# Kernel optimization log

Hardware: AMD Instinct MI355X
Metric: run time of the kernel (lower is better)

## Reference

```python
import jax, jax.numpy as jnp
import numpy as np

N, E = 50000, 800000
IN_DIM, HID, OUT, HEADS = 128, 128, 64, 4
C1 = HID // HEADS  # 32 per-head channels in gat1
NEG_SLOPE = 0.2


def _gat_conv(x, src, dst, W, a_src, a_dst, b, heads, ch):
    """PyG GATConv (inference): gather -> edge attention -> segment softmax -> scatter."""
    n = x.shape[0]
    h = (x @ W).reshape(n, heads, ch)                      # [N,H,C]
    alpha_src = jnp.einsum('nhc,hc->nh', h, a_src)         # [N,H]
    alpha_dst = jnp.einsum('nhc,hc->nh', h, a_dst)         # [N,H]
    e = jax.nn.leaky_relu(alpha_src[src] + alpha_dst[dst], NEG_SLOPE)  # [E,H]
    m = jax.ops.segment_max(e, dst, num_segments=n)        # per-target max (stable softmax)
    e = jnp.exp(e - m[dst])
    denom = jax.ops.segment_sum(e, dst, num_segments=n)
    alpha = e / (denom[dst] + 1e-16)                       # [E,H]
    out = jax.ops.segment_sum(h[src] * alpha[:, :, None], dst, num_segments=n)  # [N,H,C]
    return out.reshape(n, heads * ch) + b


def setup_inputs() -> dict:
    key = jax.random.key(0)
    ks = jax.random.split(key, 16)
    x = jax.random.normal(ks[0], (N, IN_DIM), dtype=jnp.float32)
    edge_index = jax.random.randint(ks[1], (2, E), 0, N, dtype=jnp.int64)
    s = lambda fan_in: 1.0 / np.sqrt(fan_in)
    return {
        'x': x,
        'edge_index': edge_index,
        'W1': jax.random.normal(ks[2], (IN_DIM, HEADS * C1), jnp.float32) * s(IN_DIM),
        'a_src1': jax.random.normal(ks[3], (HEADS, C1), jnp.float32) * s(C1),
        'a_dst1': jax.random.normal(ks[4], (HEADS, C1), jnp.float32) * s(C1),
        'b1': jnp.zeros((HID,), jnp.float32),
        'W2': jax.random.normal(ks[5], (HID, OUT), jnp.float32) * s(HID),
        'a_src2': jax.random.normal(ks[6], (1, OUT), jnp.float32) * s(OUT),
        'a_dst2': jax.random.normal(ks[7], (1, OUT), jnp.float32) * s(OUT),
        'b2': jnp.zeros((OUT,), jnp.float32),
        'pw1': jax.random.normal(ks[8], (OUT, OUT), jnp.float32) * s(OUT),
        'pb1': jnp.zeros((OUT,), jnp.float32),
        'pw2': jax.random.normal(ks[9], (OUT, OUT), jnp.float32) * s(OUT),
        'pb2': jnp.zeros((OUT,), jnp.float32),
    }


def reference(x, edge_index, W1, a_src1, a_dst1, b1, W2, a_src2, a_dst2, b2, pw1, pb1, pw2, pb2):
    n = x.shape[0]
    # PyG GATConv add_self_loops=True
    loops = jnp.arange(n, dtype=edge_index.dtype)
    src = jnp.concatenate([edge_index[0], loops])
    dst = jnp.concatenate([edge_index[1], loops])
    h = jax.nn.elu(_gat_conv(x, src, dst, W1, a_src1, a_dst1, b1, HEADS, C1))
    h = jax.nn.elu(_gat_conv(h, src, dst, W2, a_src2, a_dst2, b2, 1, OUT))
    # origin_proj: Linear -> ReLU -> Linear
    h = jax.nn.relu(h @ pw1 + pb1)
    return h @ pw2 + pb2
```

## Files before the change

kernel.cpp:

```cpp
#include <hip/hip_runtime.h>
#include <math.h>

#define N_NODES 50000
#define N_EDGES 800000
#define ET (N_EDGES + N_NODES)
#define IN_DIM 128
#define HID 128
#define OUT_DIM 64
#define BW 64
#define NBUCK ((N_NODES + BW - 1) / BW)
#define NBLK 256
#define EPB 3328
#define NT64 ((N_NODES + 63) / 64)
#define NT32 ((N_NODES + 31) / 32)

typedef __attribute__((ext_vector_type(8))) short bf16x8;
typedef __attribute__((ext_vector_type(4))) float f32x4;

__device__ __forceinline__ float lrelu(float x){ return x >= 0.f ? x : 0.2f * x; }
__device__ __forceinline__ float eluf(float x){ return x > 0.f ? x : expm1f(x); }
__device__ __forceinline__ unsigned f2bf(float f){
    unsigned u = __float_as_uint(f);
    return (u + 0x7fffu + ((u >> 16) & 1u)) >> 16;
}
__device__ __forceinline__ float bflo(unsigned u){ return __uint_as_float(u << 16); }
__device__ __forceinline__ float bfhi(unsigned u){ return __uint_as_float(u & 0xffff0000u); }

__global__ __launch_bounds__(256) void k_count(const int* __restrict__ dst,
                                               int* __restrict__ C,
                                               int* __restrict__ bsum2)
{
    __shared__ int cnt[NBUCK];
    const int tid = threadIdx.x, blk = blockIdx.x;
    for (int i = tid; i < NBUCK; i += 256) cnt[i] = 0;
    __syncthreads();
    #pragma unroll
    for (int j = 0; j < EPB / 256; j++) {
        const int e = blk * EPB + j * 256 + tid;
        if (e < ET) {
            const int d = (e < N_EDGES) ? dst[e] : (e - N_EDGES);
            atomicAdd(&cnt[d >> 6], 1);
        }
    }
    __syncthreads();
    for (int b = tid; b < NBUCK; b += 256) {
        const int v = cnt[b];
        C[b * NBLK + blk] = v;
        if (v) atomicAdd(&bsum2[b], v);
    }
}

__global__ __launch_bounds__(1024) void k_bscanB(const int* __restrict__ bsum2, int* __restrict__ boff2)
{
    __shared__ int part[1024];
    const int t = threadIdx.x;
    int v = (t < NBUCK) ? bsum2[t] : 0;
    part[t] = v;
    __syncthreads();
    #pragma unroll
    for (int d = 1; d < 1024; d <<= 1) {
        int add = (t >= d) ? part[t - d] : 0;
        __syncthreads();
        part[t] += add;
        __syncthreads();
    }
    if (t < NBUCK) boff2[t] = part[t] - v;
    if (t == 0) boff2[NBUCK] = ET;
}

__global__ __launch_bounds__(256) void k_cscanC(const int* __restrict__ C,
                                                const int* __restrict__ boff2,
                                                int* __restrict__ Cs)
{
    __shared__ int part[256];
    const int t = threadIdx.x, b = blockIdx.x;
    int v = C[b * NBLK + t];
    part[t] = v;
    __syncthreads();
    #pragma unroll
    for (int d = 1; d < 256; d <<= 1) {
        int add = (t >= d) ? part[t - d] : 0;
        __syncthreads();
        part[t] += add;
        __syncthreads();
    }
    Cs[b * NBLK + t] = boff2[b] + part[t] - v;
}

__global__ __launch_bounds__(256, 2) void k_gemm1_part2(
    const float* __restrict__ x, const float* __restrict__ W1,
    const float* __restrict__ a_s, const float* __restrict__ a_d,
    unsigned* __restrict__ h1b, float* __restrict__ as1, float* __restrict__ ad1,
    const int* __restrict__ src, const int* __restrict__ dst,
    const int* __restrict__ Cs, uint2* __restrict__ part)
{
    __shared__ unsigned smem[128 * 68 + 64 * 68];
    const int tid = threadIdx.x;

    if (blockIdx.x < NT64) {
        unsigned* sWt = smem;
        unsigned* sxb = smem + 128 * 68;
        const int wave = tid >> 6;
        const int lane = tid & 63;
        const int ll   = lane & 15;
        const int quad = lane >> 4;
        const int n0 = blockIdx.x * 64;

        for (int idx = tid; idx < 8192; idx += 256) {
            const int n = idx & 127, kp = idx >> 7;
            const float w0 = W1[(2 * kp) * 128 + n];
            const float w1 = W1[(2 * kp + 1) * 128 + n];
            sWt[n * 68 + kp] = f2bf(w0) | (f2bf(w1) << 16);
        }
        for (int idx = tid; idx < 4096; idx += 256) {
            const int node = idx >> 6, kp = idx & 63;
            const int n = n0 + node;
            unsigned pk = 0;
            if (n < N_NODES) {
                const float x0 = x[n * 128 + 2 * kp];
                const float x1 = x[n * 128 + 2 * kp + 1];
                pk = f2bf(x0) | (f2bf(x1) << 16);
            }
            sxb[node * 68 + kp] = pk;
        }
        __syncthreads();

        f32x4 acc[8];
        #pragma unroll
        for (int t = 0; t < 8; t++) acc[t] = (f32x4){0.f, 0.f, 0.f, 0.f};

        #pragma unroll
        for (int kk = 0; kk < 4; kk++) {
            const int kpo = 16 * kk + 4 * quad;
            const bf16x8 a = *(const bf16x8*)&sxb[(16 * wave + ll) * 68 + kpo];
            #pragma unroll
            for (int t = 0; t < 8; t++) {
                const bf16x8 b = *(const bf16x8*)&sWt[(16 * t + ll) * 68 + kpo];
                acc[t] = __builtin_amdgcn_mfma_f32_16x16x32_bf16(a, b, acc[t], 0, 0, 0);
            }
        }

        float as_v[8], ad_v[8];
        #pragma unroll
        for (int t = 0; t < 8; t++) { as_v[t] = a_s[16 * t + ll]; ad_v[t] = a_d[16 * t + ll]; }
        unsigned short* h1u = (unsigned short*)h1b;
        #pragma unroll
        for (int r = 0; r < 4; r++) {
            const int n = n0 + 16 * wave + 4 * quad + r;
            float ps0 = acc[0][r] * as_v[0] + acc[1][r] * as_v[1];
            float ps1 = acc[2][r] * as_v[2] + acc[3][r] * as_v[3];
            float ps2 = acc[4][r] * as_v[4] + acc[5][r] * as_v[5];
            float ps3 = acc[6][r] * as_v[6] + acc[7][r] * as_v[7];
            float pd0 = acc[0][r] * ad_v[0] + acc[1][r] * ad_v[1];
            float pd1 = acc[2][r] * ad_v[2] + acc[3][r] * ad_v[3];
            float pd2 = acc[4][r] * ad_v[4] + acc[5][r] * ad_v[5];
            float pd3 = acc[6][r] * ad_v[6] + acc[7][r] * ad_v[7];
            #pragma unroll
            for (int off = 1; off < 16; off <<= 1) {
                ps0 += __shfl_xor(ps0, off); ps1 += __shfl_xor(ps1, off);
                ps2 += __shfl_xor(ps2, off); ps3 += __shfl_xor(ps3, off);
                pd0 += __shfl_xor(pd0, off); pd1 += __shfl_xor(pd1, off);
                pd2 += __shfl_xor(pd2, off); pd3 += __shfl_xor(pd3, off);
            }
            if (n < N_NODES) {
                #pragma unroll
                for (int t = 0; t < 8; t++)
                    h1u[n * 128 + 16 * t + ll] = (unsigned short)f2bf(acc[t][r]);
                if (ll == 0) {
                    as1[n * 4 + 0] = ps0; as1[n * 4 + 1] = ps1;
                    as1[n * 4 + 2] = ps2; as1[n * 4 + 3] = ps3;
                    ad1[n * 4 + 0] = pd0; ad1[n * 4 + 1] = pd1;
                    ad1[n * 4 + 2] = pd2; ad1[n * 4 + 3] = pd3;
                }
            }
        }
    } else {
        const int blk = blockIdx.x - NT64;
        int* base = (int*)smem;
        int* cnt  = (int*)smem + NBUCK;
        for (int b = tid; b < NBUCK; b += 256) { base[b] = Cs[b * NBLK + blk]; cnt[b] = 0; }
        __syncthreads();
        #pragma unroll
        for (int j = 0; j < EPB / 256; j++) {
            const int e = blk * EPB + j * 256 + tid;
            if (e < ET) {
                int s, d;
                if (e < N_EDGES) { s = src[e]; d = dst[e]; } else { s = d = e - N_EDGES; }
                const int b = d >> 6;
                const int r = atomicAdd(&cnt[b], 1);
                part[base[b] + r] = make_uint2((unsigned)d, (unsigned)s);
            }
        }
    }
}

__global__ __launch_bounds__(256) void k_scat2(const int* __restrict__ boff2,
                                               const uint2* __restrict__ part,
                                               int* __restrict__ rowptr,
                                               int* __restrict__ csr_src)
{
    __shared__ int cnt64[BW];
    __shared__ int nbase[BW];
    const int b = blockIdx.x, tid = threadIdx.x;
    const int n0 = b * BW;
    const int lo = boff2[b], hi = boff2[b + 1];
    if (tid < BW) cnt64[tid] = 0;
    __syncthreads();
    for (int i = lo + tid; i < hi; i += 256) {
        atomicAdd(&cnt64[part[i].x & (BW - 1)], 1);
    }
    __syncthreads();
    if (tid < BW) {
        int v = cnt64[tid];
        int incl = v;
        #pragma unroll
        for (int off = 1; off < 64; off <<= 1) {
            int t2 = __shfl_up(incl, off);
            if (tid >= off) incl += t2;
        }
        const int excl = incl - v;
        nbase[tid] = excl;
        const int n = n0 + tid;
        if (n < N_NODES) rowptr[n] = lo + excl;
        cnt64[tid] = 0;
    }
    if (b == 0 && tid == 0) rowptr[N_NODES] = ET;
    __syncthreads();
    for (int i = lo + tid; i < hi; i += 256) {
        const uint2 p = part[i];
        const int dn = (int)p.x & (BW - 1);
        const int r = atomicAdd(&cnt64[dn], 1);
        csr_src[lo + nbase[dn] + r] = (int)p.y;
    }
}

__global__ __launch_bounds__(512, 4) void k_aggr1_l2(
    const int* __restrict__ rowptr, const int* __restrict__ csr_src,
    const float* __restrict__ as1, const float* __restrict__ ad1,
    const uint4* __restrict__ h1u4, const float* __restrict__ b1,
    const float* __restrict__ W2, const float* __restrict__ a_s2, const float* __restrict__ a_d2,
    unsigned* __restrict__ h2b, float* __restrict__ as2, float* __restrict__ ad2)
{
    __shared__ unsigned sWt[64 * 68];
    __shared__ unsigned sxb[32 * 68];
    const int tid = threadIdx.x;
    const int n0 = blockIdx.x * 32;

    for (int idx = tid; idx < 4096; idx += 512) {
        const int n = idx & 63, kp = idx >> 6;
        const float w0 = W2[(2 * kp) * 64 + n];
        const float w1 = W2[(2 * kp + 1) * 64 + n];
        sWt[n * 68 + kp] = f2bf(w0) | (f2bf(w1) << 16);
    }

    {
        const int dl = tid >> 4;
        const int c8 = tid & 15;
        const int hd = c8 >> 2;
        const int d = n0 + dl;
        uint4 o = make_uint4(0, 0, 0, 0);
        if (d < N_NODES) {
            const int r0 = rowptr[d], r1 = rowptr[d + 1];
            const float adv = ad1[d * 4 + hd];
            float den = 0.f;
            float acc[8];
            #pragma unroll
            for (int m = 0; m < 8; m++) acc[m] = 0.f;
            int i = r0;
            for (; i + 4 <= r1; i += 4) {
                const int s0 = csr_src[i],     s1 = csr_src[i + 1];
                const int s2 = csr_src[i + 2], s3 = csr_src[i + 3];
                const float e0 = as1[s0 * 4 + hd], e1 = as1[s1 * 4 + hd];
                const float e2 = as1[s2 * 4 + hd], e3 = as1[s3 * 4 + hd];
                const uint4 u0 = h1u4[s0 * 16 + c8];
                const uint4 u1 = h1u4[s1 * 16 + c8];
                const uint4 u2 = h1u4[s2 * 16 + c8];
                const uint4 u3 = h1u4[s3 * 16 + c8];
                const float w0 = expf(lrelu(e0 + adv));
                const float w1 = expf(lrelu(e1 + adv));
                const float w2 = expf(lrelu(e2 + adv));
                const float w3 = expf(lrelu(e3 + adv));
                den += (w0 + w1) + (w2 + w3);
                acc[0] = fmaf(bflo(u0.x), w0, acc[0]); acc[1] = fmaf(bfhi(u0.x), w0, acc[1]);
                acc[2] = fmaf(bflo(u0.y), w0, acc[2]); acc[3] = fmaf(bfhi(u0.y), w0, acc[3]);
                acc[4] = fmaf(bflo(u0.z), w0, acc[4]); acc[5] = fmaf(bfhi(u0.z), w0, acc[5]);
                acc[6] = fmaf(bflo(u0.w), w0, acc[6]); acc[7] = fmaf(bfhi(u0.w), w0, acc[7]);
                acc[0] = fmaf(bflo(u1.x), w1, acc[0]); acc[1] = fmaf(bfhi(u1.x), w1, acc[1]);
                acc[2] = fmaf(bflo(u1.y), w1, acc[2]); acc[3] = fmaf(bfhi(u1.y), w1, acc[3]);
                acc[4] = fmaf(bflo(u1.z), w1, acc[4]); acc[5] = fmaf(bfhi(u1.z), w1, acc[5]);
                acc[6] = fmaf(bflo(u1.w), w1, acc[6]); acc[7] = fmaf(bfhi(u1.w), w1, acc[7]);
                acc[0] = fmaf(bflo(u2.x), w2, acc[0]); acc[1] = fmaf(bfhi(u2.x), w2, acc[1]);
                acc[2] = fmaf(bflo(u2.y), w2, acc[2]); acc[3] = fmaf(bfhi(u2.y), w2, acc[3]);
                acc[4] = fmaf(bflo(u2.z), w2, acc[4]); acc[5] = fmaf(bfhi(u2.z), w2, acc[5]);
                acc[6] = fmaf(bflo(u2.w), w2, acc[6]); acc[7] = fmaf(bfhi(u2.w), w2, acc[7]);
                acc[0] = fmaf(bflo(u3.x), w3, acc[0]); acc[1] = fmaf(bfhi(u3.x), w3, acc[1]);
                acc[2] = fmaf(bflo(u3.y), w3, acc[2]); acc[3] = fmaf(bfhi(u3.y), w3, acc[3]);
                acc[4] = fmaf(bflo(u3.z), w3, acc[4]); acc[5] = fmaf(bfhi(u3.z), w3, acc[5]);
                acc[6] = fmaf(bflo(u3.w), w3, acc[6]); acc[7] = fmaf(bfhi(u3.w), w3, acc[7]);
            }
            for (; i < r1; ++i) {
                const int s = csr_src[i];
                const float w = expf(lrelu(as1[s * 4 + hd] + adv));
                const uint4 u = h1u4[s * 16 + c8];
                den += w;
                acc[0] = fmaf(bflo(u.x), w, acc[0]); acc[1] = fmaf(bfhi(u.x), w, acc[1]);
                acc[2] = fmaf(bflo(u.y), w, acc[2]); acc[3] = fmaf(bfhi(u.y), w, acc[3]);
                acc[4] = fmaf(bflo(u.z), w, acc[4]); acc[5] = fmaf(bfhi(u.z), w, acc[5]);
                acc[6] = fmaf(bflo(u.w), w, acc[6]); acc[7] = fmaf(bfhi(u.w), w, acc[7]);
            }
            const float inv = 1.f / (den + 1e-16f);
            const float4 bA = ((const float4*)b1)[2 * c8];
            const float4 bB = ((const float4*)b1)[2 * c8 + 1];
            const float v0 = eluf(acc[0] * inv + bA.x);
            const float v1 = eluf(acc[1] * inv + bA.y);
            const float v2 = eluf(acc[2] * inv + bA.z);
            const float v3 = eluf(acc[3] * inv + bA.w);
            const float v4 = eluf(acc[4] * inv + bB.x);
            const float v5 = eluf(acc[5] * inv + bB.y);
            const float v6 = eluf(acc[6] * inv + bB.z);
            const float v7 = eluf(acc[7] * inv + bB.w);
            o.x = f2bf(v0) | (f2bf(v1) << 16);
            o.y = f2bf(v2) | (f2bf(v3) << 16);
            o.z = f2bf(v4) | (f2bf(v5) << 16);
            o.w = f2bf(v6) | (f2bf(v7) << 16);
        }
        unsigned* dstp = &sxb[dl * 68 + 4 * c8];
        dstp[0] = o.x; dstp[1] = o.y; dstp[2] = o.z; dstp[3] = o.w;
    }
    __syncthreads();

    if (tid < 128) {
        const int wave = tid >> 6;
        const int lane = tid & 63;
        const int ll   = lane & 15;
        const int quad = lane >> 4;

        f32x4 acc[4];
        #pragma unroll
        for (int t = 0; t < 4; t++) acc[t] = (f32x4){0.f, 0.f, 0.f, 0.f};

        #pragma unroll
        for (int kk = 0; kk < 4; kk++) {
            const int kpo = 16 * kk + 4 * quad;
            const bf16x8 a = *(const bf16x8*)&sxb[(16 * wave + ll) * 68 + kpo];
            #pragma unroll
            for (int t = 0; t < 4; t++) {
                const bf16x8 b = *(const bf16x8*)&sWt[(16 * t + ll) * 68 + kpo];
                acc[t] = __builtin_amdgcn_mfma_f32_16x16x32_bf16(a, b, acc[t], 0, 0, 0);
            }
        }

        float as_v[4], ad_v[4];
        #pragma unroll
        for (int t = 0; t < 4; t++) { as_v[t] = a_s2[16 * t + ll]; ad_v[t] = a_d2[16 * t + ll]; }
        unsigned short* h2u = (unsigned short*)h2b;
        #pragma unroll
        for (int r = 0; r < 4; r++) {
            const int n = n0 + 16 * wave + 4 * quad + r;
            float ps = acc[0][r] * as_v[0] + acc[1][r] * as_v[1]
                     + acc[2][r] * as_v[2] + acc[3][r] * as_v[3];
            float pd = acc[0][r] * ad_v[0] + acc[1][r] * ad_v[1]
                     + acc[2][r] * ad_v[2] + acc[3][r] * ad_v[3];
            #pragma unroll
            for (int off = 1; off < 16; off <<= 1) {
                ps += __shfl_xor(ps, off);
                pd += __shfl_xor(pd, off);
            }
            if (n < N_NODES) {
                #pragma unroll
                for (int t = 0; t < 4; t++)
                    h2u[n * 64 + 16 * t + ll] = (unsigned short)f2bf(acc[t][r]);
                if (ll == 0) { as2[n] = ps; ad2[n] = pd; }
            }
        }
    }
}

__global__ __launch_bounds__(512, 4) void k_tail(
    const int* __restrict__ rowptr, const int* __restrict__ csr_src,
    const float* __restrict__ as2, const float* __restrict__ ad2,
    const uint4* __restrict__ h2u4, const float* __restrict__ b2,
    const float* __restrict__ pw1, const float* __restrict__ pb1,
    const float* __restrict__ pw2, const float* __restrict__ pb2,
    float* __restrict__ out)
{
    __shared__ float sW1[64 * 64];
    __shared__ float sW2[64 * 64];
    __shared__ float sosp[64][68];
    const int tid = threadIdx.x;
    const int n0 = blockIdx.x * 64;

    for (int i = tid; i < 1024; i += 512) {
        ((float4*)sW1)[i] = ((const float4*)pw1)[i];
        ((float4*)sW2)[i] = ((const float4*)pw2)[i];
    }

    {
        const int dl = tid >> 3;
        const int c8 = tid & 7;
        const int d = n0 + dl;
        float acc[8];
        #pragma unroll
        for (int m = 0; m < 8; m++) acc[m] = 0.f;
        float v0 = 0.f, v1 = 0.f, v2 = 0.f, v3 = 0.f;
        float v4 = 0.f, v5 = 0.f, v6 = 0.f, v7 = 0.f;
        if (d < N_NODES) {
            const int r0 = rowptr[d], r1 = rowptr[d + 1];
            const float adv = ad2[d];
            float den = 0.f;
            int i = r0;
            for (; i + 4 <= r1; i += 4) {
                const int s0 = csr_src[i],      s1_ = csr_src[i + 1];
                const int s2_ = csr_src[i + 2], s3_ = csr_src[i + 3];
                const float e0 = as2[s0], e1 = as2[s1_], e2 = as2[s2_], e3 = as2[s3_];
                const uint4 u0 = h2u4[s0  * 8 + c8];
                const uint4 u1 = h2u4[s1_ * 8 + c8];
                const uint4 u2 = h2u4[s2_ * 8 + c8];
                const uint4 u3 = h2u4[s3_ * 8 + c8];
                const float w0 = expf(lrelu(e0 + adv));
                const float w1 = expf(lrelu(e1 + adv));
                const float w2 = expf(lrelu(e2 + adv));
                const float w3 = expf(lrelu(e3 + adv));
                den += (w0 + w1) + (w2 + w3);
                acc[0] = fmaf(bflo(u0.x), w0, acc[0]); acc[1] = fmaf(bfhi(u0.x), w0, acc[1]);
                acc[2] = fmaf(bflo(u0.y), w0, acc[2]); acc[3] = fmaf(bfhi(u0.y), w0, acc[3]);
                acc[4] = fmaf(bflo(u0.z), w0, acc[4]); acc[5] = fmaf(bfhi(u0.z), w0, acc[5]);
                acc[6] = fmaf(bflo(u0.w), w0, acc[6]); acc[7] = fmaf(bfhi(u0.w), w0, acc[7]);
                acc[0] = fmaf(bflo(u1.x), w1, acc[0]); acc[1] = fmaf(bfhi(u1.x), w1, acc[1]);
                acc[2] = fmaf(bflo(u1.y), w1, acc[2]); acc[3] = fmaf(bfhi(u1.y), w1, acc[3]);
                acc[4] = fmaf(bflo(u1.z), w1, acc[4]); acc[5] = fmaf(bfhi(u1.z), w1, acc[5]);
                acc[6] = fmaf(bflo(u1.w), w1, acc[6]); acc[7] = fmaf(bfhi(u1.w), w1, acc[7]);
                acc[0] = fmaf(bflo(u2.x), w2, acc[0]); acc[1] = fmaf(bfhi(u2.x), w2, acc[1]);
                acc[2] = fmaf(bflo(u2.y), w2, acc[2]); acc[3] = fmaf(bfhi(u2.y), w2, acc[3]);
                acc[4] = fmaf(bflo(u2.z), w2, acc[4]); acc[5] = fmaf(bfhi(u2.z), w2, acc[5]);
                acc[6] = fmaf(bflo(u2.w), w2, acc[6]); acc[7] = fmaf(bfhi(u2.w), w2, acc[7]);
                acc[0] = fmaf(bflo(u3.x), w3, acc[0]); acc[1] = fmaf(bfhi(u3.x), w3, acc[1]);
                acc[2] = fmaf(bflo(u3.y), w3, acc[2]); acc[3] = fmaf(bfhi(u3.y), w3, acc[3]);
                acc[4] = fmaf(bflo(u3.z), w3, acc[4]); acc[5] = fmaf(bfhi(u3.z), w3, acc[5]);
                acc[6] = fmaf(bflo(u3.w), w3, acc[6]); acc[7] = fmaf(bfhi(u3.w), w3, acc[7]);
            }
            for (; i < r1; ++i) {
                const int s = csr_src[i];
                const float w = expf(lrelu(as2[s] + adv));
                const uint4 u = h2u4[s * 8 + c8];
                den += w;
                acc[0] = fmaf(bflo(u.x), w, acc[0]); acc[1] = fmaf(bfhi(u.x), w, acc[1]);
                acc[2] = fmaf(bflo(u.y), w, acc[2]); acc[3] = fmaf(bfhi(u.y), w, acc[3]);
                acc[4] = fmaf(bflo(u.z), w, acc[4]); acc[5] = fmaf(bfhi(u.z), w, acc[5]);
                acc[6] = fmaf(bflo(u.w), w, acc[6]); acc[7] = fmaf(bfhi(u.w), w, acc[7]);
            }
            const float inv = 1.f / (den + 1e-16f);
            const float4 bA = ((const float4*)b2)[2 * c8];
            const float4 bB = ((const float4*)b2)[2 * c8 + 1];
            v0 = eluf(acc[0] * inv + bA.x);
            v1 = eluf(acc[1] * inv + bA.y);
            v2 = eluf(acc[2] * inv + bA.z);
            v3 = eluf(acc[3] * inv + bA.w);
            v4 = eluf(acc[4] * inv + bB.x);
            v5 = eluf(acc[5] * inv + bB.y);
            v6 = eluf(acc[6] * inv + bB.z);
            v7 = eluf(acc[7] * inv + bB.w);
        }
        *(float4*)&sosp[dl][8 * c8]     = make_float4(v0, v1, v2, v3);
        *(float4*)&sosp[dl][8 * c8 + 4] = make_float4(v4, v5, v6, v7);
    }
    __syncthreads();

    const int cg = tid & 15;
    const int ng = tid >> 4;
    const float4 pb1_4 = ((const float4*)pb1)[cg];
    const float4 pb2_4 = ((const float4*)pb2)[cg];
    float4 p[2];
    #pragma unroll
    for (int m = 0; m < 2; m++) p[m] = pb1_4;
    #pragma unroll 8
    for (int k = 0; k < 64; k++) {
        const float4 w = *(const float4*)&sW1[k * 64 + 4 * cg];
        #pragma unroll
        for (int m = 0; m < 2; m++) {
            const float xv = sosp[2 * ng + m][k];
            p[m].x = fmaf(xv, w.x, p[m].x);
            p[m].y = fmaf(xv, w.y, p[m].y);
            p[m].z = fmaf(xv, w.z, p[m].z);
            p[m].w = fmaf(xv, w.w, p[m].w);
        }
    }
    __syncthreads();

    #pragma unroll
    for (int m = 0; m < 2; m++) {
        p[m].x = fmaxf(p[m].x, 0.f); p[m].y = fmaxf(p[m].y, 0.f);
        p[m].z = fmaxf(p[m].z, 0.f); p[m].w = fmaxf(p[m].w, 0.f);
        *(float4*)&sosp[2 * ng + m][4 * cg] = p[m];
    }
    __syncthreads();

    float4 o[2];
    #pragma unroll
    for (int m = 0; m < 2; m++) o[m] = pb2_4;
    #pragma unroll 8
    for (int k = 0; k < 64; k++) {
        const float4 w = *(const float4*)&sW2[k * 64 + 4 * cg];
        #pragma unroll
        for (int m = 0; m < 2; m++) {
            const float xv = sosp[2 * ng + m][k];
            o[m].x = fmaf(xv, w.x, o[m].x);
            o[m].y = fmaf(xv, w.y, o[m].y);
            o[m].z = fmaf(xv, w.z, o[m].z);
            o[m].w = fmaf(xv, w.w, o[m].w);
        }
    }
    #pragma unroll
    for (int m = 0; m < 2; m++) {
        const int n = n0 + 2 * ng + m;
        if (n < N_NODES) ((float4*)out)[n * 16 + cg] = o[m];
    }
}

extern "C" void kernel_launch(void* const* d_in, const int* in_sizes, int n_in,
                              void* d_out, int out_size, void* d_ws, size_t ws_size,
                              hipStream_t stream)
{
    const float* x      = (const float*)d_in[0];
    const int*   ei     = (const int*)d_in[1];
    const int*   src    = ei;
    const int*   dst    = ei + N_EDGES;
    const float* W1     = (const float*)d_in[2];
    const float* a_src1 = (const float*)d_in[3];
    const float* a_dst1 = (const float*)d_in[4];
    const float* b1     = (const float*)d_in[5];
    const float* W2     = (const float*)d_in[6];
    const float* a_src2 = (const float*)d_in[7];
    const float* a_dst2 = (const float*)d_in[8];
    const float* b2     = (const float*)d_in[9];
    const float* pw1    = (const float*)d_in[10];
    const float* pb1    = (const float*)d_in[11];
    const float* pw2    = (const float*)d_in[12];
    const float* pb2    = (const float*)d_in[13];

    uint2* part  = (uint2*)d_ws;
    int* ibase   = (int*)(part + ET);
    int* rowptr  = ibase;
    int* C       = rowptr + 50004;
    int* Cs      = C + 200192;
    int* bsum2   = Cs + 200192;
    int* boff2   = bsum2 + 784;
    int* csr_src = boff2 + 784;
    unsigned* h1b = (unsigned*)(csr_src + 850000);
    unsigned* h2b = h1b + 3200000;
    float* fws   = (float*)(h2b + 1600000);
    float* as1   = fws;
    float* ad1   = as1 + 200000;
    float* as2   = ad1 + 200000;
    float* ad2   = as2 + 50000;

    hipMemsetAsync(bsum2, 0, NBUCK * sizeof(int), stream);
    k_count<<<NBLK, 256, 0, stream>>>(dst, C, bsum2);
    k_bscanB<<<1, 1024, 0, stream>>>(bsum2, boff2);
    k_cscanC<<<NBUCK, 256, 0, stream>>>(C, boff2, Cs);

    k_gemm1_part2<<<NT64 + NBLK, 256, 0, stream>>>(x, W1, a_src1, a_dst1,
                                                   h1b, as1, ad1,
                                                   src, dst, Cs, part);
    k_scat2<<<NBUCK, 256, 0, stream>>>(boff2, part, rowptr, csr_src);

    k_aggr1_l2<<<NT32, 512, 0, stream>>>(rowptr, csr_src, as1, ad1,
                                         (const uint4*)h1b, b1,
                                         W2, a_src2, a_dst2, h2b, as2, ad2);

    k_tail<<<NT64, 512, 0, stream>>>(rowptr, csr_src, as2, ad2,
                                     (const uint4*)h2b, b2,
                                     pw1, pb1, pw2, pb2, (float*)d_out);
}
```

Measured before the change: 243.2 us.

## Split layer-1 aggregation from layer-2 GEMM into separate kernels

Unfuses the layer-1 attention aggregation from the layer-2 projection. The aggregation now runs as its own 256-thread kernel, 16 nodes per block with no shared memory, and writes ELU-activated bf16 features to a new workspace buffer. A separate MFMA kernel reads that buffer to do the W2 projection and the attention logits. The aim is to raise occupancy for the latency-bound gather and avoid idle waves during the GEMM. The cost is an extra launch plus a 12.8 MB write and reread of the intermediate.

```diff
diff --git a/kernel.cpp b/kernel.cpp
--- a/kernel.cpp
+++ b/kernel.cpp
@@ -12,7 +12,6 @@
 #define NBLK 256
 #define EPB 3328
 #define NT64 ((N_NODES + 63) / 64)
-#define NT32 ((N_NODES + 31) / 32)
 
 typedef __attribute__((ext_vector_type(8))) short bf16x8;
 typedef __attribute__((ext_vector_type(4))) float f32x4;
@@ -234,144 +233,149 @@
     }
 }
 
-__global__ __launch_bounds__(512, 4) void k_aggr1_l2(
+__global__ __launch_bounds__(256) void k_aggr1(
     const int* __restrict__ rowptr, const int* __restrict__ csr_src,
     const float* __restrict__ as1, const float* __restrict__ ad1,
     const uint4* __restrict__ h1u4, const float* __restrict__ b1,
+    unsigned* __restrict__ hEb)
+{
+    const int d  = blockIdx.x * 16 + (threadIdx.x >> 4);
+    const int c8 = threadIdx.x & 15;
+    const int hd = c8 >> 2;
+    const int r0 = rowptr[d], r1 = rowptr[d + 1];
+    const float adv = ad1[d * 4 + hd];
+    float den = 0.f;
+    float acc[8];
+    #pragma unroll
+    for (int m = 0; m < 8; m++) acc[m] = 0.f;
+    int i = r0;
+    for (; i + 4 <= r1; i += 4) {
+        const int s0 = csr_src[i],     s1 = csr_src[i + 1];
+        const int s2 = csr_src[i + 2], s3 = csr_src[i + 3];
+        const float e0 = as1[s0 * 4 + hd], e1 = as1[s1 * 4 + hd];
+        const float e2 = as1[s2 * 4 + hd], e3 = as1[s3 * 4 + hd];
+        const uint4 u0 = h1u4[s0 * 16 + c8];
+        const uint4 u1 = h1u4[s1 * 16 + c8];
+        const uint4 u2 = h1u4[s2 * 16 + c8];
+        const uint4 u3 = h1u4[s3 * 16 + c8];
+        const float w0 = expf(lrelu(e0 + adv));
+        const float w1 = expf(lrelu(e1 + adv));
+        const float w2 = expf(lrelu(e2 + adv));
+        const float w3 = expf(lrelu(e3 + adv));
+        den += (w0 + w1) + (w2 + w3);
+        acc[0] = fmaf(bflo(u0.x), w0, acc[0]); acc[1] = fmaf(bfhi(u0.x), w0, acc[1]);
+        acc[2] = fmaf(bflo(u0.y), w0, acc[2]); acc[3] = fmaf(bfhi(u0.y), w0, acc[3]);
+        acc[4] = fmaf(bflo(u0.z), w0, acc[4]); acc[5] = fmaf(bfhi(u0.z), w0, acc[5]);
+        acc[6] = fmaf(bflo(u0.w), w0, acc[6]); acc[7] = fmaf(bfhi(u0.w), w0, acc[7]);
+        acc[0] = fmaf(bflo(u1.x), w1, acc[0]); acc[1] = fmaf(bfhi(u1.x), w1, acc[1]);
+        acc[2] = fmaf(bflo(u1.y), w1, acc[2]); acc[3] = fmaf(bfhi(u1.y), w1, acc[3]);
+        acc[4] = fmaf(bflo(u1.z), w1, acc[4]); acc[5] = fmaf(bfhi(u1.z), w1, acc[5]);
+        acc[6] = fmaf(bflo(u1.w), w1, acc[6]); acc[7] = fmaf(bfhi(u1.w), w1, acc[7]);
+        acc[0] = fmaf(bflo(u2.x), w2, acc[0]); acc[1] = fmaf(bfhi(u2.x), w2, acc[1]);
+        acc[2] = fmaf(bflo(u2.y), w2, acc[2]); acc[3] = fmaf(bfhi(u2.y), w2, acc[3]);
+        acc[4] = fmaf(bflo(u2.z), w2, acc[4]); acc[5] = fmaf(bfhi(u2.z), w2, acc[5]);
+        acc[6] = fmaf(bflo(u2.w), w2, acc[6]); acc[7] = fmaf(bfhi(u2.w), w2, acc[7]);
+        acc[0] = fmaf(bflo(u3.x), w3, acc[0]); acc[1] = fmaf(bfhi(u3.x), w3, acc[1]);
+        acc[2] = fmaf(bflo(u3.y), w3, acc[2]); acc[3] = fmaf(bfhi(u3.y), w3, acc[3]);
+        acc[4] = fmaf(bflo(u3.z), w3, acc[4]); acc[5] = fmaf(bfhi(u3.z), w3, acc[5]);
+        acc[6] = fmaf(bflo(u3.w), w3, acc[6]); acc[7] = fmaf(bfhi(u3.w), w3, acc[7]);
+    }
+    for (; i < r1; ++i) {
+        const int s = csr_src[i];
+        const float w = expf(lrelu(as1[s * 4 + hd] + adv));
+        const uint4 u = h1u4[s * 16 + c8];
+        den += w;
+        acc[0] = fmaf(bflo(u.x), w, acc[0]); acc[1] = fmaf(bfhi(u.x), w, acc[1]);
+        acc[2] = fmaf(bflo(u.y), w, acc[2]); acc[3] = fmaf(bfhi(u.y), w, acc[3]);
+        acc[4] = fmaf(bflo(u.z), w, acc[4]); acc[5] = fmaf(bfhi(u.z), w, acc[5]);
+        acc[6] = fmaf(bflo(u.w), w, acc[6]); acc[7] = fmaf(bfhi(u.w), w, acc[7]);
+    }
+    const float inv = 1.f / (den + 1e-16f);
+    const float4 bA = ((const float4*)b1)[2 * c8];
+    const float4 bB = ((const float4*)b1)[2 * c8 + 1];
+    const float v0 = eluf(acc[0] * inv + bA.x);
+    const float v1 = eluf(acc[1] * inv + bA.y);
+    const float v2 = eluf(acc[2] * inv + bA.z);
+    const float v3 = eluf(acc[3] * inv + bA.w);
+    const float v4 = eluf(acc[4] * inv + bB.x);
+    const float v5 = eluf(acc[5] * inv + bB.y);
+    const float v6 = eluf(acc[6] * inv + bB.z);
+    const float v7 = eluf(acc[7] * inv + bB.w);
+    uint4 o;
+    o.x = f2bf(v0) | (f2bf(v1) << 16);
+    o.y = f2bf(v2) | (f2bf(v3) << 16);
+    o.z = f2bf(v4) | (f2bf(v5) << 16);
+    o.w = f2bf(v6) | (f2bf(v7) << 16);
+    ((uint4*)hEb)[d * 16 + c8] = o;
+}
+
+__global__ __launch_bounds__(256, 4) void k_layer2(
+    const unsigned* __restrict__ hEb,
     const float* __restrict__ W2, const float* __restrict__ a_s2, const float* __restrict__ a_d2,
     unsigned* __restrict__ h2b, float* __restrict__ as2, float* __restrict__ ad2)
 {
     __shared__ unsigned sWt[64 * 68];
-    __shared__ unsigned sxb[32 * 68];
+    __shared__ unsigned sxb[64 * 68];
     const int tid = threadIdx.x;
-    const int n0 = blockIdx.x * 32;
-
-    for (int idx = tid; idx < 4096; idx += 512) {
+    const int wave = tid >> 6;
+    const int lane = tid & 63;
+    const int ll   = lane & 15;
+    const int quad = lane >> 4;
+    const int n0 = blockIdx.x * 64;
+
+    for (int idx = tid; idx < 4096; idx += 256) {
         const int n = idx & 63, kp = idx >> 6;
         const float w0 = W2[(2 * kp) * 64 + n];
         const float w1 = W2[(2 * kp + 1) * 64 + n];
         sWt[n * 68 + kp] = f2bf(w0) | (f2bf(w1) << 16);
     }
-
-    {
-        const int dl = tid >> 4;
-        const int c8 = tid & 15;
-        const int hd = c8 >> 2;
-        const int d = n0 + dl;
-        uint4 o = make_uint4(0, 0, 0, 0);
-        if (d < N_NODES) {
-            const int r0 = rowptr[d], r1 = rowptr[d + 1];
-            const float adv = ad1[d * 4 + hd];
-            float den = 0.f;
-            float acc[8];
+    const uint4* hE4 = (const uint4*)hEb;
+    for (int idx = tid; idx < 1024; idx += 256) {
+        const int node = idx >> 4, q = idx & 15;
+        const int n = n0 + node;
+        uint4 pk = make_uint4(0, 0, 0, 0);
+        if (n < N_NODES) pk = hE4[n * 16 + q];
+        unsigned* dstp = &sxb[node * 68 + 4 * q];
+        dstp[0] = pk.x; dstp[1] = pk.y; dstp[2] = pk.z; dstp[3] = pk.w;
+    }
+    __syncthreads();
+
+    f32x4 acc[4];
+    #pragma unroll
+    for (int t = 0; t < 4; t++) acc[t] = (f32x4){0.f, 0.f, 0.f, 0.f};
+
+    #pragma unroll
+    for (int kk = 0; kk < 4; kk++) {
+        const int kpo = 16 * kk + 4 * quad;
+        const bf16x8 a = *(const bf16x8*)&sxb[(16 * wave + ll) * 68 + kpo];
+        #pragma unroll
+        for (int t = 0; t < 4; t++) {
+            const bf16x8 b = *(const bf16x8*)&sWt[(16 * t + ll) * 68 + kpo];
+            acc[t] = __builtin_amdgcn_mfma_f32_16x16x32_bf16(a, b, acc[t], 0, 0, 0);
+        }
+    }
+
+    float as_v[4], ad_v[4];
+    #pragma unroll
+    for (int t = 0; t < 4; t++) { as_v[t] = a_s2[16 * t + ll]; ad_v[t] = a_d2[16 * t + ll]; }
+    unsigned short* h2u = (unsigned short*)h2b;
+    #pragma unroll
+    for (int r = 0; r < 4; r++) {
+        const int n = n0 + 16 * wave + 4 * quad + r;
+        float ps = acc[0][r] * as_v[0] + acc[1][r] * as_v[1]
+                 + acc[2][r] * as_v[2] + acc[3][r] * as_v[3];
+        float pd = acc[0][r] * ad_v[0] + acc[1][r] * ad_v[1]
+                 + acc[2][r] * ad_v[2] + acc[3][r] * ad_v[3];
+        #pragma unroll
+        for (int off = 1; off < 16; off <<= 1) {
+            ps += __shfl_xor(ps, off);
+            pd += __shfl_xor(pd, off);
+        }
+        if (n < N_NODES) {
             #pragma unroll
-            for (int m = 0; m < 8; m++) acc[m] = 0.f;
-            int i = r0;
-            for (; i + 4 <= r1; i += 4) {
-                const int s0 = csr_src[i],     s1 = csr_src[i + 1];
-                const int s2 = csr_src[i + 2], s3 = csr_src[i + 3];
-                const float e0 = as1[s0 * 4 + hd], e1 = as1[s1 * 4 + hd];
-                const float e2 = as1[s2 * 4 + hd], e3 = as1[s3 * 4 + hd];
-                const uint4 u0 = h1u4[s0 * 16 + c8];
-                const uint4 u1 = h1u4[s1 * 16 + c8];
-                const uint4 u2 = h1u4[s2 * 16 + c8];
-                const uint4 u3 = h1u4[s3 * 16 + c8];
-                const float w0 = expf(lrelu(e0 + adv));
-                const float w1 = expf(lrelu(e1 + adv));
-                const float w2 = expf(lrelu(e2 + adv));
-                const float w3 = expf(lrelu(e3 + adv));
-                den += (w0 + w1) + (w2 + w3);
-                acc[0] = fmaf(bflo(u0.x), w0, acc[0]); acc[1] = fmaf(bfhi(u0.x), w0, acc[1]);
-                acc[2] = fmaf(bflo(u0.y), w0, acc[2]); acc[3] = fmaf(bfhi(u0.y), w0, acc[3]);
-                acc[4] = fmaf(bflo(u0.z), w0, acc[4]); acc[5] = fmaf(bfhi(u0.z), w0, acc[5]);
-                acc[6] = fmaf(bflo(u0.w), w0, acc[6]); acc[7] = fmaf(bfhi(u0.w), w0, acc[7]);
-                acc[0] = fmaf(bflo(u1.x), w1, acc[0]); acc[1] = fmaf(bfhi(u1.x), w1, acc[1]);
-                acc[2] = fmaf(bflo(u1.y), w1, acc[2]); acc[3] = fmaf(bfhi(u1.y), w1, acc[3]);
-                acc[4] = fmaf(bflo(u1.z), w1, acc[4]); acc[5] = fmaf(bfhi(u1.z), w1, acc[5]);
-                acc[6] = fmaf(bflo(u1.w), w1, acc[6]); acc[7] = fmaf(bfhi(u1.w), w1, acc[7]);
-                acc[0] = fmaf(bflo(u2.x), w2, acc[0]); acc[1] = fmaf(bfhi(u2.x), w2, acc[1]);
-                acc[2] = fmaf(bflo(u2.y), w2, acc[2]); acc[3] = fmaf(bfhi(u2.y), w2, acc[3]);
-                acc[4] = fmaf(bflo(u2.z), w2, acc[4]); acc[5] = fmaf(bfhi(u2.z), w2, acc[5]);
-                acc[6] = fmaf(bflo(u2.w), w2, acc[6]); acc[7] = fmaf(bfhi(u2.w), w2, acc[7]);
-                acc[0] = fmaf(bflo(u3.x), w3, acc[0]); acc[1] = fmaf(bfhi(u3.x), w3, acc[1]);
-                acc[2] = fmaf(bflo(u3.y), w3, acc[2]); acc[3] = fmaf(bfhi(u3.y), w3, acc[3]);
-                acc[4] = fmaf(bflo(u3.z), w3, acc[4]); acc[5] = fmaf(bfhi(u3.z), w3, acc[5]);
-                acc[6] = fmaf(bflo(u3.w), w3, acc[6]); acc[7] = fmaf(bfhi(u3.w), w3, acc[7]);
-            }
-            for (; i < r1; ++i) {
-                const int s = csr_src[i];
-                const float w = expf(lrelu(as1[s * 4 + hd] + adv));
-                const uint4 u = h1u4[s * 16 + c8];
-                den += w;
-                acc[0] = fmaf(bflo(u.x), w, acc[0]); acc[1] = fmaf(bfhi(u.x), w, acc[1]);
-                acc[2] = fmaf(bflo(u.y), w, acc[2]); acc[3] = fmaf(bfhi(u.y), w, acc[3]);
-                acc[4] = fmaf(bflo(u.z), w, acc[4]); acc[5] = fmaf(bfhi(u.z), w, acc[5]);
-                acc[6] = fmaf(bflo(u.w), w, acc[6]); acc[7] = fmaf(bfhi(u.w), w, acc[7]);
-            }
-            const float inv = 1.f / (den + 1e-16f);
-            const float4 bA = ((const float4*)b1)[2 * c8];
-            const float4 bB = ((const float4*)b1)[2 * c8 + 1];
-            const float v0 = eluf(acc[0] * inv + bA.x);
-            const float v1 = eluf(acc[1] * inv + bA.y);
-            const float v2 = eluf(acc[2] * inv + bA.z);
-            const float v3 = eluf(acc[3] * inv + bA.w);
-            const float v4 = eluf(acc[4] * inv + bB.x);
-            const float v5 = eluf(acc[5] * inv + bB.y);
-            const float v6 = eluf(acc[6] * inv + bB.z);
-            const float v7 = eluf(acc[7] * inv + bB.w);
-            o.x = f2bf(v0) | (f2bf(v1) << 16);
-            o.y = f2bf(v2) | (f2bf(v3) << 16);
-            o.z = f2bf(v4) | (f2bf(v5) << 16);
-            o.w = f2bf(v6) | (f2bf(v7) << 16);
-        }
-        unsigned* dstp = &sxb[dl * 68 + 4 * c8];
-        dstp[0] = o.x; dstp[1] = o.y; dstp[2] = o.z; dstp[3] = o.w;
-    }
-    __syncthreads();
-
-    if (tid < 128) {
-        const int wave = tid >> 6;
-        const int lane = tid & 63;
-        const int ll   = lane & 15;
-        const int quad = lane >> 4;
-
-        f32x4 acc[4];
-        #pragma unroll
-        for (int t = 0; t < 4; t++) acc[t] = (f32x4){0.f, 0.f, 0.f, 0.f};
-
-        #pragma unroll
-        for (int kk = 0; kk < 4; kk++) {
-            const int kpo = 16 * kk + 4 * quad;
-            const bf16x8 a = *(const bf16x8*)&sxb[(16 * wave + ll) * 68 + kpo];
-            #pragma unroll
-            for (int t = 0; t < 4; t++) {
-                const bf16x8 b = *(const bf16x8*)&sWt[(16 * t + ll) * 68 + kpo];
-                acc[t] = __builtin_amdgcn_mfma_f32_16x16x32_bf16(a, b, acc[t], 0, 0, 0);
-            }
-        }
-
-        float as_v[4], ad_v[4];
-        #pragma unroll
-        for (int t = 0; t < 4; t++) { as_v[t] = a_s2[16 * t + ll]; ad_v[t] = a_d2[16 * t + ll]; }
-        unsigned short* h2u = (unsigned short*)h2b;
-        #pragma unroll
-        for (int r = 0; r < 4; r++) {
-            const int n = n0 + 16 * wave + 4 * quad + r;
-            float ps = acc[0][r] * as_v[0] + acc[1][r] * as_v[1]
-                     + acc[2][r] * as_v[2] + acc[3][r] * as_v[3];
-            float pd = acc[0][r] * ad_v[0] + acc[1][r] * ad_v[1]
-                     + acc[2][r] * ad_v[2] + acc[3][r] * ad_v[3];
-            #pragma unroll
-            for (int off = 1; off < 16; off <<= 1) {
-                ps += __shfl_xor(ps, off);
-                pd += __shfl_xor(pd, off);
-            }
-            if (n < N_NODES) {
-                #pragma unroll
-                for (int t = 0; t < 4; t++)
-                    h2u[n * 64 + 16 * t + ll] = (unsigned short)f2bf(acc[t][r]);
-                if (ll == 0) { as2[n] = ps; ad2[n] = pd; }
-            }
+            for (int t = 0; t < 4; t++)
+                h2u[n * 64 + 16 * t + ll] = (unsigned short)f2bf(acc[t][r]);
+            if (ll == 0) { as2[n] = ps; ad2[n] = pd; }
         }
     }
 }
@@ -551,7 +555,8 @@
     float* fws   = (float*)(h2b + 1600000);
     float* as1   = fws;
     float* ad1   = as1 + 200000;
-    float* as2   = ad1 + 200000;
+    unsigned* hEb = (unsigned*)(ad1 + 200000);
+    float* as2   = (float*)(hEb + 3200000);
     float* ad2   = as2 + 50000;
 
     hipMemsetAsync(bsum2, 0, NBUCK * sizeof(int), stream);
@@ -564,9 +569,10 @@
                                                    src, dst, Cs, part);
     k_scat2<<<NBUCK, 256, 0, stream>>>(boff2, part, rowptr, csr_src);
 
-    k_aggr1_l2<<<NT32, 512, 0, stream>>>(rowptr, csr_src, as1, ad1,
-                                         (const uint4*)h1b, b1,
-                                         W2, a_src2, a_dst2, h2b, as2, ad2);
+    k_aggr1<<<N_NODES / 16, 256, 0, stream>>>(rowptr, csr_src, as1, ad1,
+                                              (const uint4*)h1b, b1, hEb);
+
+    k_layer2<<<NT64, 256, 0, stream>>>(hEb, W2, a_src2, a_dst2, h2b, as2, ad2);
 
     k_tail<<<NT64, 512, 0, stream>>>(rowptr, csr_src, as2, ad2,
                                      (const uint4*)h2b, b2,
```

Result: slower. 250.5 us (+3.0%).
